# Kernel tuning notes

Measured on AMD Instinct MI355X. Metric: run time of the kernel, lower is better.

The kernel has to match this reference:

```python
import jax, jax.numpy as jnp
import numpy as np

NUM_CLASSES = 2
LOG2_NC = float(np.log2(NUM_CLASSES))


def _conv(x, w, b=None):
    # NCHW conv, stride 1, SAME padding (kernel 3 pad 1 or kernel 1 pad 0)
    y = jax.lax.conv_general_dilated(x, w, (1, 1), 'SAME',
                                     dimension_numbers=('NCHW', 'OIHW', 'NCHW'))
    if b is not None:
        y = y + b[None, :, None, None]
    return y


def _uncertainty_map(ds):
    # entropy over class dim, thresholded to {0,1}
    logp = jax.nn.log_softmax(ds, axis=1)            # [B,C,H,W]
    prob = jnp.exp(logp)
    # torch uses log2(prob + 1e-6); replicate exactly
    ent = -jnp.sum(prob * jnp.log2(prob + 1e-6), axis=1) / LOG2_NC  # [B,H,W]
    return (ent >= 0.001).astype(jnp.float32)


def _unob(tar, amap):
    # vectorized UnoB with S=3: interior pixels with tar!=0 get pro=0 unless
    # 4*tar == sum of the 4-neighborhood (i.e. locally constant label)
    t = tar  # [B,H,W] int
    nb = t[:, 2:, 1:-1] + t[:, :-2, 1:-1] + t[:, 1:-1, 2:] + t[:, 1:-1, :-2]
    center = t[:, 1:-1, 1:-1]
    inner_pro = jnp.where((center != 0) & (4 * center != nb), 0.0, 1.0)
    pro = jnp.ones_like(amap)
    pro = pro.at[:, 1:-1, 1:-1].set(inner_pro)
    return amap * pro


def setup_inputs() -> dict:
    key = jax.random.key(0)
    ks = jax.random.split(key, 6)
    B, C, H, W = 8, 128, 128, 128
    return {
        'x': jax.random.normal(ks[0], (B, C, H, W), jnp.float32),
        'skip': jax.random.normal(ks[1], (B, C, H, W), jnp.float32),
        'tar': jax.random.randint(ks[2], (B, 1, H, W), 0, NUM_CLASSES, jnp.int64)
            if jax.config.jax_enable_x64 else
            jax.random.randint(ks[2], (B, 1, H, W), 0, NUM_CLASSES).astype(jnp.int32),
        'W1': jax.random.normal(ks[3], (128, 256, 3, 3), jnp.float32) * 0.05,
        'b1': jnp.zeros((128,), jnp.float32),
        'W2': jax.random.normal(ks[4], (128, 128, 3, 3), jnp.float32) * 0.05,
        'b2': jnp.zeros((128,), jnp.float32),
        'Wds': jax.random.normal(ks[5], (NUM_CLASSES, 128, 1, 1), jnp.float32) * 0.05,
    }


def reference(x, skip, tar, W1, b1, W2, b2, Wds):
    h = jnp.concatenate([x, skip], axis=1)            # [B,2*dim,H,W]
    h = jax.nn.leaky_relu(_conv(h, W1, b1), 0.01)     # [B,dim,H,W]
    h = jax.nn.leaky_relu(_conv(h, W2, b2), 0.01)
    ds = _conv(h, Wds)                                # [B,num_classes,H,W]
    amap = _uncertainty_map(ds)                       # [B,H,W]
    amap = _unob(tar[:, 0], amap)                     # UnoB refinement, S=3
    return h, ds, amap
```

## Files before the change

kernel.cpp:

```cpp
#include <hip/hip_runtime.h>

typedef float f32x16 __attribute__((ext_vector_type(16)));
typedef short bf16x8 __attribute__((ext_vector_type(8)));
typedef unsigned int u32;

static __device__ __forceinline__ unsigned short f2bf(float f) {
  union { float f; unsigned int u; } v;
  v.f = f;
  return (unsigned short)((v.u + 0x7FFFu + ((v.u >> 16) & 1u)) >> 16);
}

static __device__ __forceinline__ void gl_lds16(const unsigned short* g,
                                                unsigned short* l) {
  __builtin_amdgcn_global_load_lds(
      (const __attribute__((address_space(1))) u32*)g,
      (__attribute__((address_space(3))) u32*)l, 16, 0, 0);
}

__global__ __launch_bounds__(256) void convert_weights(
    const float* __restrict__ W1, const float* __restrict__ W2,
    unsigned short* __restrict__ W1b, unsigned short* __restrict__ W2b,
    unsigned short* __restrict__ zp) {
  if (blockIdx.x == 1728) {
    uint4* z = (uint4*)zp;
    z[threadIdx.x] = make_uint4(0, 0, 0, 0);
    z[256 + threadIdx.x] = make_uint4(0, 0, 0, 0);
    return;
  }
  int i = blockIdx.x * 256 + threadIdx.x;
  if (i < 294912) {
    int e = i & 7, co = (i >> 3) & 127, r = i >> 10;
    int tap = r % 9, pc = r / 9;
    int ci = (pc >> 1) * 16 + (pc & 1) * 8 + e;
    W1b[i] = f2bf(W1[(co * 256 + ci) * 9 + tap]);
  } else {
    int j = i - 294912;
    if (j < 147456) {
      int e = j & 7, co = (j >> 3) & 127, r = j >> 10;
      int tap = r % 9, pc = r / 9;
      int ci = (pc >> 1) * 16 + (pc & 1) * 8 + e;
      W2b[j] = f2bf(W2[(co * 128 + ci) * 9 + tap]);
    }
  }
}

__global__ __launch_bounds__(256) void transpose_to_bf16(
    const float* __restrict__ src, unsigned short* __restrict__ dst, int cigb) {
  int row = blockIdx.x;
  int b = row >> 7, y = row & 127;
  const float* s = src + (long)b * 128 * 16384 + (long)y * 128;
  for (int it = 0; it < 8; ++it) {
    int u = it * 256 + (int)threadIdx.x;
    int cig = u >> 7, px = u & 127;
    unsigned short pk[8];
#pragma unroll
    for (int e = 0; e < 8; ++e)
      pk[e] = f2bf(s[(long)(cig * 8 + e) * 16384 + px]);
    uint4 vv;
    vv.x = (unsigned)pk[0] | ((unsigned)pk[1] << 16);
    vv.y = (unsigned)pk[2] | ((unsigned)pk[3] << 16);
    vv.z = (unsigned)pk[4] | ((unsigned)pk[5] << 16);
    vv.w = (unsigned)pk[6] | ((unsigned)pk[7] << 16);
    *(uint4*)(&dst[(((long)row * 32 + cigb + cig) * 130 + px + 1) * 8]) = vv;
  }
  if (cigb == 0 && threadIdx.x < 64) {
    int g = threadIdx.x >> 1;
    long col = (threadIdx.x & 1) * 129L;
    *(uint4*)(&dst[(((long)row * 32 + g) * 130 + col) * 8]) = make_uint4(0, 0, 0, 0);
  }
}

#define IPL 520
template <int CIN, bool FUSE_DS>
__global__ __launch_bounds__(512) void conv3x3(
    const unsigned short* __restrict__ src,
    const unsigned short* __restrict__ wt,
    const float* __restrict__ bias,
    const unsigned short* __restrict__ zp,
    unsigned short* __restrict__ dst_bf16,
    float* __restrict__ dst_f32,
    const float* __restrict__ wds,
    const int* __restrict__ tar,
    float* __restrict__ ds,
    float* __restrict__ amap) {
  constexpr int CPG = CIN / 8;
  constexpr int NC = CIN / 16;
  __shared__ unsigned short in_tile[2][2 * IPL * 8];
  __shared__ unsigned short wt_tile[2][2304 * 8];
  __shared__ float sb[128];
  __shared__ float w0s[128], w1s[128];
  __shared__ float sc[4 * 2 * 2 * 32];

  const int tid = threadIdx.x;
  const int b = blockIdx.x >> 6;
  const int y0 = (blockIdx.x & 63) * 2;
  const int lane = tid & 63, wave = tid >> 6;
  const int wco = wave & 1, wpx = wave >> 1;
  const int l31 = lane & 31, kh = lane >> 5;
  const int rowoff = wpx >> 1, p0 = (wpx & 1) * 64;

  if (tid < 128) {
    sb[tid] = bias[tid];
    if constexpr (FUSE_DS) {
      w0s[tid] = wds[tid];
      w1s[tid] = wds[128 + tid];
    }
  }

  const int shy = wave >> 1, sp = wave & 1;
  const int sgy = y0 - 1 + shy;
  const bool sok = (sgy >= 0 && sgy < 128);
  const unsigned short* srow =
      sok ? src + ((long)((b * 128 + sgy) * CPG) + sp) * 1040 : zp;
  const int tseg = tid >> 1, thx = 128 + (tid & 1);
  const int tp = tseg & 1, thy = tseg >> 1;
  const int tgy = y0 - 1 + thy;

#define STAGE_WT(cic, bufi)                                                   \
  {                                                                           \
    const unsigned short* wslab = wt + (long)(cic)*18432;                     \
    for (int o = wave; o < 36; o += 8)                                        \
      gl_lds16(wslab + (o * 64 + lane) * 8,                                   \
               &wt_tile[bufi][(size_t)(o * 64) * 8]);                         \
  }

#define STAGE_BULK(cic, bufi)                                                 \
  {                                                                           \
    _Pragma("unroll") for (int j = 0; j < 2; ++j)                             \
        gl_lds16(srow + (sok ? ((long)(cic)*2 * 1040 + (j * 64 + lane) * 8)   \
                             : (long)(lane * 8)),                             \
                 &in_tile[bufi][(size_t)(sp * IPL + shy * 130 + j * 64) * 8]);\
  }

#define LOAD_TAIL(cic, v)                                                     \
  {                                                                           \
    if (tid < 16 && tgy >= 0 && tgy < 128)                                    \
      v = *(const uint4*)(src +                                               \
                          ((long)((b * 128 + tgy) * CPG) + (cic)*2 + tp) *    \
                              1040 +                                          \
                          thx * 8);                                           \
  }

#define WRITE_TAIL(bufi, v)                                                   \
  {                                                                           \
    if (tid < 16)                                                             \
      *(uint4*)(&in_tile[bufi][(size_t)(tp * IPL + thy * 130 + thx) * 8]) = v;\
  }

  f32x16 acc[2][2] = {};

  {
    uint4 tv = make_uint4(0, 0, 0, 0);
    LOAD_TAIL(0, tv);
    STAGE_WT(0, 0);
    STAGE_BULK(0, 0);
    WRITE_TAIL(0, tv);
  }
  __syncthreads();

  for (int cic = 0; cic < NC; ++cic) {
    const int cur = cic & 1, nb = cur ^ 1;
    const bool more = (cic + 1 < NC);
    uint4 tl = make_uint4(0, 0, 0, 0);
    if (more) {
      LOAD_TAIL(cic + 1, tl);
      STAGE_WT(cic + 1, nb);
      STAGE_BULK(cic + 1, nb);
    }
    __builtin_amdgcn_sched_barrier(0);
    const unsigned short* it = in_tile[cur];
    const unsigned short* wl = wt_tile[cur];
    const size_t ibase = (size_t)(kh * IPL) * 8;
    const size_t wbase = (size_t)(kh * 1152) * 8;
#pragma unroll
    for (int ky = 0; ky < 3; ++ky) {
      const int hy = ky + rowoff;
#pragma unroll
      for (int kx = 0; kx < 3; ++kx) {
        const int t = ky * 3 + kx;
        bf16x8 a0 = *(const bf16x8*)(&wl[wbase + (size_t)(t * 128 + wco * 64 + l31) * 8]);
        bf16x8 a1 = *(const bf16x8*)(&wl[wbase + (size_t)(t * 128 + wco * 64 + 32 + l31) * 8]);
        bf16x8 b0 = *(const bf16x8*)(&it[ibase + (size_t)(hy * 130 + p0 + l31 + kx) * 8]);
        bf16x8 b1 = *(const bf16x8*)(&it[ibase + (size_t)(hy * 130 + p0 + 32 + l31 + kx) * 8]);
        acc[0][0] = __builtin_amdgcn_mfma_f32_32x32x16_bf16(a0, b0, acc[0][0], 0, 0, 0);
        acc[0][1] = __builtin_amdgcn_mfma_f32_32x32x16_bf16(a0, b1, acc[0][1], 0, 0, 0);
        acc[1][0] = __builtin_amdgcn_mfma_f32_32x32x16_bf16(a1, b0, acc[1][0], 0, 0, 0);
        acc[1][1] = __builtin_amdgcn_mfma_f32_32x32x16_bf16(a1, b1, acc[1][1], 0, 0, 0);
      }
    }
    if (more) WRITE_TAIL(nb, tl);
    __syncthreads();
  }

  const int gyo = y0 + rowoff;
  float pd[2][2] = {};
#pragma unroll
  for (int fc = 0; fc < 2; ++fc) {
#pragma unroll
    for (int fp = 0; fp < 2; ++fp) {
      const int px = p0 + fp * 32 + l31;
      if constexpr (!FUSE_DS) {
#pragma unroll
        for (int rg = 0; rg < 4; ++rg) {
          const int co0 = wco * 64 + fc * 32 + rg * 8 + kh * 4;
          unsigned short pk[4];
#pragma unroll
          for (int q = 0; q < 4; ++q) {
            float v = acc[fc][fp][rg * 4 + q] + sb[co0 + q];
            v = v > 0.f ? v : 0.01f * v;
            pk[q] = f2bf(v);
          }
          uint2 o;
          o.x = (unsigned)pk[0] | ((unsigned)pk[1] << 16);
          o.y = (unsigned)pk[2] | ((unsigned)pk[3] << 16);
          *(uint2*)(&dst_bf16[(((long)(b * 128 + gyo) * 16 + (co0 >> 3)) * 130 + px + 1) * 8 +
                              kh * 4]) = o;
        }
      } else {
#pragma unroll
        for (int rg = 0; rg < 4; ++rg) {
          const int co0 = wco * 64 + fc * 32 + rg * 8 + kh * 4;
          float4 wv0 = *(const float4*)(&w0s[co0]);
          float4 wv1 = *(const float4*)(&w1s[co0]);
#pragma unroll
          for (int q = 0; q < 4; ++q) {
            float v = acc[fc][fp][rg * 4 + q] + sb[co0 + q];
            v = v > 0.f ? v : 0.01f * v;
            dst_f32[((long)(b * 128 + co0 + q) << 14) + (gyo << 7) + px] = v;
            float wq0 = (q == 0) ? wv0.x : (q == 1) ? wv0.y : (q == 2) ? wv0.z : wv0.w;
            float wq1 = (q == 0) ? wv1.x : (q == 1) ? wv1.y : (q == 2) ? wv1.z : wv1.w;
            pd[fp][0] += wq0 * v;
            pd[fp][1] += wq1 * v;
          }
        }
      }
    }
  }

  if constexpr (!FUSE_DS) {
    if (tid < 64) {
      int row = tid >> 5, g = (tid >> 1) & 15;
      long col = (tid & 1) * 129L;
      *(uint4*)(&dst_bf16[(((long)(b * 128 + y0 + row) * 16 + g) * 130 + col) * 8]) =
          make_uint4(0, 0, 0, 0);
    }
  } else {
#pragma unroll
    for (int fp = 0; fp < 2; ++fp)
#pragma unroll
      for (int c = 0; c < 2; ++c)
        pd[fp][c] += __shfl_xor(pd[fp][c], 32, 64);
    if (wco == 1 && kh == 0) {
#pragma unroll
      for (int fp = 0; fp < 2; ++fp)
#pragma unroll
        for (int c = 0; c < 2; ++c)
          sc[((wpx * 2 + fp) * 2 + c) * 32 + l31] = pd[fp][c];
    }
    __syncthreads();
    if (wco == 0 && kh == 0) {
      const int* tb = tar + (long)b * 16384;
#pragma unroll
      for (int fp = 0; fp < 2; ++fp) {
        const int px = p0 + fp * 32 + l31;
        float a0 = pd[fp][0] + sc[((wpx * 2 + fp) * 2 + 0) * 32 + l31];
        float a1 = pd[fp][1] + sc[((wpx * 2 + fp) * 2 + 1) * 32 + l31];
        ds[((long)b * 2) * 16384 + (gyo << 7) + px] = a0;
        ds[((long)b * 2 + 1) * 16384 + (gyo << 7) + px] = a1;
        float m = fmaxf(a0, a1);
        float e0 = expf(a0 - m), e1 = expf(a1 - m);
        float s = e0 + e1;
        float p0f = e0 / s, p1f = e1 / s;
        float ent = -(p0f * log2f(p0f + 1e-6f) + p1f * log2f(p1f + 1e-6f));
        float un = ent >= 0.001f ? 1.f : 0.f;
        float pro = 1.f;
        if (gyo > 0 && gyo < 127 && px > 0 && px < 127) {
          int c = tb[(gyo << 7) + px];
          if (c != 0) {
            int nb2 = tb[((gyo - 1) << 7) + px] + tb[((gyo + 1) << 7) + px] +
                      tb[(gyo << 7) + px - 1] + tb[(gyo << 7) + px + 1];
            if (4 * c != nb2) pro = 0.f;
          }
        }
        amap[((long)(b * 128 + gyo) << 7) + px] = un * pro;
      }
    }
  }
#undef STAGE_WT
#undef STAGE_BULK
#undef LOAD_TAIL
#undef WRITE_TAIL
}

extern "C" void kernel_launch(void* const* d_in, const int* in_sizes, int n_in,
                              void* d_out, int out_size, void* d_ws, size_t ws_size,
                              hipStream_t stream) {
  const float* x    = (const float*)d_in[0];
  const float* skip = (const float*)d_in[1];
  const int*   tar  = (const int*)d_in[2];
  const float* W1   = (const float*)d_in[3];
  const float* b1   = (const float*)d_in[4];
  const float* W2   = (const float*)d_in[5];
  const float* b2   = (const float*)d_in[6];
  const float* Wds  = (const float*)d_in[7];

  float* out_h  = (float*)d_out;
  float* out_ds = out_h + 16777216;
  float* out_am = out_ds + 262144;

  unsigned short* W1b = (unsigned short*)d_ws;
  unsigned short* W2b = W1b + 294912;
  unsigned short* zp  = W2b + 147456;
  unsigned short* h1  = (unsigned short*)((char*)d_ws + (1u << 20));

  unsigned short* h0 = (unsigned short*)d_out;

  convert_weights<<<1729, 256, 0, stream>>>(W1, W2, W1b, W2b, zp);
  transpose_to_bf16<<<1024, 256, 0, stream>>>(x, h0, 0);
  transpose_to_bf16<<<1024, 256, 0, stream>>>(skip, h0, 16);
  conv3x3<256, false><<<512, 512, 0, stream>>>(h0, W1b, b1, zp, h1, nullptr,
                                               nullptr, nullptr, nullptr, nullptr);
  conv3x3<128, true><<<512, 512, 0, stream>>>(h1, W2b, b2, zp, nullptr, out_h,
                                              Wds, tar, out_ds, out_am);
}
```

Before: 163.8 us.

## Shrink conv tiles to one row per block and stream weights from global

The conv3x3 kernel now handles one output row per 256-thread block, with a 1024-block grid instead of 512 blocks of 512 threads. Weights are no longer staged through shared memory; each lane reads its weight fragments straight from global (L2) with a one-ky-ahead register prefetch. This cuts LDS use to allow several blocks per CU (launch bounds 256,3) and drops the weight-staging traffic and its barrier cost. In exchange every block re-reads the weights from cache, input halo rows are reused less (3 rows loaded per output row instead of 4 per 2), and register pressure from the prefetched fragments rises.

```diff
diff --git a/kernel.cpp b/kernel.cpp
--- a/kernel.cpp
+++ b/kernel.cpp
@@ -70,9 +70,8 @@
   }
 }
 
-#define IPL 520
 template <int CIN, bool FUSE_DS>
-__global__ __launch_bounds__(512) void conv3x3(
+__global__ __launch_bounds__(256, 3) void conv3x3(
     const unsigned short* __restrict__ src,
     const unsigned short* __restrict__ wt,
     const float* __restrict__ bias,
@@ -85,19 +84,18 @@
     float* __restrict__ amap) {
   constexpr int CPG = CIN / 8;
   constexpr int NC = CIN / 16;
-  __shared__ unsigned short in_tile[2][2 * IPL * 8];
-  __shared__ unsigned short wt_tile[2][2304 * 8];
+  __shared__ unsigned short in_tile[2][6 * 130 * 8];
   __shared__ float sb[128];
   __shared__ float w0s[128], w1s[128];
-  __shared__ float sc[4 * 2 * 2 * 32];
+  __shared__ float sc[2 * 2 * 2 * 32];
 
   const int tid = threadIdx.x;
-  const int b = blockIdx.x >> 6;
-  const int y0 = (blockIdx.x & 63) * 2;
+  const int b = blockIdx.x >> 7;
+  const int y0 = blockIdx.x & 127;
   const int lane = tid & 63, wave = tid >> 6;
   const int wco = wave & 1, wpx = wave >> 1;
   const int l31 = lane & 31, kh = lane >> 5;
-  const int rowoff = wpx >> 1, p0 = (wpx & 1) * 64;
+  const int p0 = wpx * 64;
 
   if (tid < 128) {
     sb[tid] = bias[tid];
@@ -107,44 +105,42 @@
     }
   }
 
-  const int shy = wave >> 1, sp = wave & 1;
-  const int sgy = y0 - 1 + shy;
-  const bool sok = (sgy >= 0 && sgy < 128);
-  const unsigned short* srow =
-      sok ? src + ((long)((b * 128 + sgy) * CPG) + sp) * 1040 : zp;
-  const int tseg = tid >> 1, thx = 128 + (tid & 1);
-  const int tp = tseg & 1, thy = tseg >> 1;
-  const int tgy = y0 - 1 + thy;
-
-#define STAGE_WT(cic, bufi)                                                   \
-  {                                                                           \
-    const unsigned short* wslab = wt + (long)(cic)*18432;                     \
-    for (int o = wave; o < 36; o += 8)                                        \
-      gl_lds16(wslab + (o * 64 + lane) * 8,                                   \
-               &wt_tile[bufi][(size_t)(o * 64) * 8]);                         \
-  }
-
-#define STAGE_BULK(cic, bufi)                                                 \
-  {                                                                           \
-    _Pragma("unroll") for (int j = 0; j < 2; ++j)                             \
-        gl_lds16(srow + (sok ? ((long)(cic)*2 * 1040 + (j * 64 + lane) * 8)   \
-                             : (long)(lane * 8)),                             \
-                 &in_tile[bufi][(size_t)(sp * IPL + shy * 130 + j * 64) * 8]);\
-  }
-
-#define LOAD_TAIL(cic, v)                                                     \
-  {                                                                           \
-    if (tid < 16 && tgy >= 0 && tgy < 128)                                    \
-      v = *(const uint4*)(src +                                               \
-                          ((long)((b * 128 + tgy) * CPG) + (cic)*2 + tp) *    \
-                              1040 +                                          \
-                          thx * 8);                                           \
-  }
-
-#define WRITE_TAIL(bufi, v)                                                   \
-  {                                                                           \
-    if (tid < 16)                                                             \
-      *(uint4*)(&in_tile[bufi][(size_t)(tp * IPL + thy * 130 + thx) * 8]) = v;\
+#define STAGE_BULK(cic, bufi)                                                  \
+  {                                                                            \
+    _Pragma("unroll") for (int j = 0; j < 3; ++j) {                            \
+      int o = wave + j * 4;                                                    \
+      int seg = o >> 1, half = o & 1;                                          \
+      int p = (seg >= 3) ? 1 : 0, hy = seg - p * 3;                            \
+      int gy = y0 - 1 + hy;                                                    \
+      const unsigned short* g =                                                \
+          (gy >= 0 && gy < 128)                                                \
+              ? src + ((size_t)((b * 128 + gy) * CPG) + (cic)*2 + p) * 1040 +  \
+                    (half * 64 + lane) * 8                                     \
+              : zp + lane * 8;                                                 \
+      gl_lds16(g, &in_tile[bufi][(size_t)(seg * 130 + half * 64) * 8]);        \
+    }                                                                          \
+  }
+
+#define LOAD_TAIL(cic, v)                                                      \
+  {                                                                            \
+    if (tid < 12) {                                                            \
+      int s_ = tid >> 1, p_ = (s_ >= 3) ? 1 : 0, hy_ = s_ - p_ * 3;            \
+      int cx_ = 128 + (tid & 1);                                               \
+      int gy_ = y0 - 1 + hy_;                                                  \
+      if (gy_ >= 0 && gy_ < 128)                                               \
+        v = *(const uint4*)(src +                                              \
+                            ((size_t)((b * 128 + gy_) * CPG) + (cic)*2 + p_) * \
+                                1040 +                                         \
+                            cx_ * 8);                                          \
+    }                                                                          \
+  }
+
+#define WRITE_TAIL(bufi, v)                                                    \
+  {                                                                            \
+    if (tid < 12) {                                                            \
+      int s_ = tid >> 1, cx_ = 128 + (tid & 1);                                \
+      *(uint4*)(&in_tile[bufi][(size_t)(s_ * 130 + cx_) * 8]) = v;             \
+    }                                                                          \
   }
 
   f32x16 acc[2][2] = {};
@@ -152,47 +148,58 @@
   {
     uint4 tv = make_uint4(0, 0, 0, 0);
     LOAD_TAIL(0, tv);
-    STAGE_WT(0, 0);
     STAGE_BULK(0, 0);
     WRITE_TAIL(0, tv);
   }
   __syncthreads();
 
+  const unsigned short* wlane = wt + (size_t)kh * 9216 + (size_t)(wco * 64 + l31) * 8;
+
   for (int cic = 0; cic < NC; ++cic) {
-    const int cur = cic & 1, nb = cur ^ 1;
+    const int cur = cic & 1, nbuf = cur ^ 1;
     const bool more = (cic + 1 < NC);
     uint4 tl = make_uint4(0, 0, 0, 0);
     if (more) {
       LOAD_TAIL(cic + 1, tl);
-      STAGE_WT(cic + 1, nb);
-      STAGE_BULK(cic + 1, nb);
+      STAGE_BULK(cic + 1, nbuf);
     }
     __builtin_amdgcn_sched_barrier(0);
+    const unsigned short* wl = wlane + (size_t)cic * 18432;
     const unsigned short* it = in_tile[cur];
-    const unsigned short* wl = wt_tile[cur];
-    const size_t ibase = (size_t)(kh * IPL) * 8;
-    const size_t wbase = (size_t)(kh * 1152) * 8;
+    bf16x8 a0[3], a1[3];
+#pragma unroll
+    for (int t = 0; t < 3; ++t) {
+      a0[t] = *(const bf16x8*)(wl + t * 1024);
+      a1[t] = *(const bf16x8*)(wl + t * 1024 + 256);
+    }
 #pragma unroll
     for (int ky = 0; ky < 3; ++ky) {
-      const int hy = ky + rowoff;
+      bf16x8 n0[3], n1[3];
+      if (ky < 2) {
+#pragma unroll
+        for (int t = 0; t < 3; ++t) {
+          n0[t] = *(const bf16x8*)(wl + (ky * 3 + 3 + t) * 1024);
+          n1[t] = *(const bf16x8*)(wl + (ky * 3 + 3 + t) * 1024 + 256);
+        }
+      }
 #pragma unroll
       for (int kx = 0; kx < 3; ++kx) {
-        const int t = ky * 3 + kx;
-        bf16x8 a0 = *(const bf16x8*)(&wl[wbase + (size_t)(t * 128 + wco * 64 + l31) * 8]);
-        bf16x8 a1 = *(const bf16x8*)(&wl[wbase + (size_t)(t * 128 + wco * 64 + 32 + l31) * 8]);
-        bf16x8 b0 = *(const bf16x8*)(&it[ibase + (size_t)(hy * 130 + p0 + l31 + kx) * 8]);
-        bf16x8 b1 = *(const bf16x8*)(&it[ibase + (size_t)(hy * 130 + p0 + 32 + l31 + kx) * 8]);
-        acc[0][0] = __builtin_amdgcn_mfma_f32_32x32x16_bf16(a0, b0, acc[0][0], 0, 0, 0);
-        acc[0][1] = __builtin_amdgcn_mfma_f32_32x32x16_bf16(a0, b1, acc[0][1], 0, 0, 0);
-        acc[1][0] = __builtin_amdgcn_mfma_f32_32x32x16_bf16(a1, b0, acc[1][0], 0, 0, 0);
-        acc[1][1] = __builtin_amdgcn_mfma_f32_32x32x16_bf16(a1, b1, acc[1][1], 0, 0, 0);
-      }
-    }
-    if (more) WRITE_TAIL(nb, tl);
+        bf16x8 b0 = *(const bf16x8*)(&it[(size_t)(kh * 390 + ky * 130 + p0 + l31 + kx) * 8]);
+        bf16x8 b1 = *(const bf16x8*)(&it[(size_t)(kh * 390 + ky * 130 + p0 + 32 + l31 + kx) * 8]);
+        acc[0][0] = __builtin_amdgcn_mfma_f32_32x32x16_bf16(a0[kx], b0, acc[0][0], 0, 0, 0);
+        acc[0][1] = __builtin_amdgcn_mfma_f32_32x32x16_bf16(a0[kx], b1, acc[0][1], 0, 0, 0);
+        acc[1][0] = __builtin_amdgcn_mfma_f32_32x32x16_bf16(a1[kx], b0, acc[1][0], 0, 0, 0);
+        acc[1][1] = __builtin_amdgcn_mfma_f32_32x32x16_bf16(a1[kx], b1, acc[1][1], 0, 0, 0);
+      }
+      if (ky < 2) {
+#pragma unroll
+        for (int t = 0; t < 3; ++t) { a0[t] = n0[t]; a1[t] = n1[t]; }
+      }
+    }
+    if (more) WRITE_TAIL(nbuf, tl);
     __syncthreads();
   }
 
-  const int gyo = y0 + rowoff;
   float pd[2][2] = {};
 #pragma unroll
   for (int fc = 0; fc < 2; ++fc) {
@@ -213,7 +220,7 @@
           uint2 o;
           o.x = (unsigned)pk[0] | ((unsigned)pk[1] << 16);
           o.y = (unsigned)pk[2] | ((unsigned)pk[3] << 16);
-          *(uint2*)(&dst_bf16[(((long)(b * 128 + gyo) * 16 + (co0 >> 3)) * 130 + px + 1) * 8 +
+          *(uint2*)(&dst_bf16[(((long)(b * 128 + y0) * 16 + (co0 >> 3)) * 130 + px + 1) * 8 +
                               kh * 4]) = o;
         }
       } else {
@@ -226,7 +233,7 @@
           for (int q = 0; q < 4; ++q) {
             float v = acc[fc][fp][rg * 4 + q] + sb[co0 + q];
             v = v > 0.f ? v : 0.01f * v;
-            dst_f32[((long)(b * 128 + co0 + q) << 14) + (gyo << 7) + px] = v;
+            dst_f32[((long)(b * 128 + co0 + q) << 14) + (y0 << 7) + px] = v;
             float wq0 = (q == 0) ? wv0.x : (q == 1) ? wv0.y : (q == 2) ? wv0.z : wv0.w;
             float wq1 = (q == 0) ? wv1.x : (q == 1) ? wv1.y : (q == 2) ? wv1.z : wv1.w;
             pd[fp][0] += wq0 * v;
@@ -238,10 +245,10 @@
   }
 
   if constexpr (!FUSE_DS) {
-    if (tid < 64) {
-      int row = tid >> 5, g = (tid >> 1) & 15;
+    if (tid < 32) {
+      int g = tid >> 1;
       long col = (tid & 1) * 129L;
-      *(uint4*)(&dst_bf16[(((long)(b * 128 + y0 + row) * 16 + g) * 130 + col) * 8]) =
+      *(uint4*)(&dst_bf16[(((long)(b * 128 + y0) * 16 + g) * 130 + col) * 8]) =
           make_uint4(0, 0, 0, 0);
     }
   } else {
@@ -265,8 +272,8 @@
         const int px = p0 + fp * 32 + l31;
         float a0 = pd[fp][0] + sc[((wpx * 2 + fp) * 2 + 0) * 32 + l31];
         float a1 = pd[fp][1] + sc[((wpx * 2 + fp) * 2 + 1) * 32 + l31];
-        ds[((long)b * 2) * 16384 + (gyo << 7) + px] = a0;
-        ds[((long)b * 2 + 1) * 16384 + (gyo << 7) + px] = a1;
+        ds[((long)b * 2) * 16384 + (y0 << 7) + px] = a0;
+        ds[((long)b * 2 + 1) * 16384 + (y0 << 7) + px] = a1;
         float m = fmaxf(a0, a1);
         float e0 = expf(a0 - m), e1 = expf(a1 - m);
         float s = e0 + e1;
@@ -274,19 +281,18 @@
         float ent = -(p0f * log2f(p0f + 1e-6f) + p1f * log2f(p1f + 1e-6f));
         float un = ent >= 0.001f ? 1.f : 0.f;
         float pro = 1.f;
-        if (gyo > 0 && gyo < 127 && px > 0 && px < 127) {
-          int c = tb[(gyo << 7) + px];
+        if (y0 > 0 && y0 < 127 && px > 0 && px < 127) {
+          int c = tb[(y0 << 7) + px];
           if (c != 0) {
-            int nb2 = tb[((gyo - 1) << 7) + px] + tb[((gyo + 1) << 7) + px] +
-                      tb[(gyo << 7) + px - 1] + tb[(gyo << 7) + px + 1];
+            int nb2 = tb[((y0 - 1) << 7) + px] + tb[((y0 + 1) << 7) + px] +
+                      tb[(y0 << 7) + px - 1] + tb[(y0 << 7) + px + 1];
             if (4 * c != nb2) pro = 0.f;
           }
         }
-        amap[((long)(b * 128 + gyo) << 7) + px] = un * pro;
-      }
-    }
-  }
-#undef STAGE_WT
+        amap[((long)(b * 128 + y0) << 7) + px] = un * pro;
+      }
+    }
+  }
 #undef STAGE_BULK
 #undef LOAD_TAIL
 #undef WRITE_TAIL
@@ -318,8 +324,8 @@
   convert_weights<<<1729, 256, 0, stream>>>(W1, W2, W1b, W2b, zp);
   transpose_to_bf16<<<1024, 256, 0, stream>>>(x, h0, 0);
   transpose_to_bf16<<<1024, 256, 0, stream>>>(skip, h0, 16);
-  conv3x3<256, false><<<512, 512, 0, stream>>>(h0, W1b, b1, zp, h1, nullptr,
-                                               nullptr, nullptr, nullptr, nullptr);
-  conv3x3<128, true><<<512, 512, 0, stream>>>(h1, W2b, b2, zp, nullptr, out_h,
-                                              Wds, tar, out_ds, out_am);
-}
+  conv3x3<256, false><<<1024, 256, 0, stream>>>(h0, W1b, b1, zp, h1, nullptr,
+                                                nullptr, nullptr, nullptr, nullptr);
+  conv3x3<128, true><<<1024, 256, 0, stream>>>(h1, W2b, b2, zp, nullptr, out_h,
+                                               Wds, tar, out_ds, out_am);
+}
```

Result: slower. 192.9 us (+17.8%).

## Use 4-wave blocks with larger per-wave tiles and single-buffered weight staging

Applied to the files above, without the earlier changes.

The conv3x3 kernel drops from 8 waves to 4 waves per block, and each wave now computes a full 128-pixel row (a 2x4 MFMA tile instead of 2x2). This doubles B-fragment reuse per A load and cuts redundant LDS reads. Weights are now staged into a single LDS buffer each iteration, and the input keeps its double buffer. Synchronisation uses explicit vmcnt/lgkmcnt waits and raw barriers. The aim is to reduce LDS traffic and shared-memory footprint so two blocks fit per CU, at the cost of doubling accumulator registers. Weight loads are no longer prefetched ahead, which may expose global latency.

```diff
diff --git a/kernel.cpp b/kernel.cpp
--- a/kernel.cpp
+++ b/kernel.cpp
@@ -16,6 +16,12 @@
       (const __attribute__((address_space(1))) u32*)g,
       (__attribute__((address_space(3))) u32*)l, 16, 0, 0);
 }
+
+#define VMCNT4 asm volatile("s_waitcnt vmcnt(4)" ::: "memory")
+#define VMCNT0 asm volatile("s_waitcnt vmcnt(0)" ::: "memory")
+#define LGKM0 asm volatile("s_waitcnt lgkmcnt(0)" ::: "memory")
+#define BAR __builtin_amdgcn_s_barrier()
+#define SCHEDB __builtin_amdgcn_sched_barrier(0)
 
 __global__ __launch_bounds__(256) void convert_weights(
     const float* __restrict__ W1, const float* __restrict__ W2,
@@ -70,9 +76,8 @@
   }
 }
 
-#define IPL 520
 template <int CIN, bool FUSE_DS>
-__global__ __launch_bounds__(512) void conv3x3(
+__global__ __launch_bounds__(256, 2) void conv3x3(
     const unsigned short* __restrict__ src,
     const unsigned short* __restrict__ wt,
     const float* __restrict__ bias,
@@ -85,19 +90,18 @@
     float* __restrict__ amap) {
   constexpr int CPG = CIN / 8;
   constexpr int NC = CIN / 16;
-  __shared__ unsigned short in_tile[2][2 * IPL * 8];
-  __shared__ unsigned short wt_tile[2][2304 * 8];
+  __shared__ unsigned short in_tile[2][1040 * 8];
+  __shared__ unsigned short wt_tile[2304 * 8];
   __shared__ float sb[128];
   __shared__ float w0s[128], w1s[128];
-  __shared__ float sc[4 * 2 * 2 * 32];
+  __shared__ float sc[2 * 4 * 2 * 32];
 
   const int tid = threadIdx.x;
   const int b = blockIdx.x >> 6;
   const int y0 = (blockIdx.x & 63) * 2;
   const int lane = tid & 63, wave = tid >> 6;
-  const int wco = wave & 1, wpx = wave >> 1;
+  const int wco = wave & 1, wrow = wave >> 1;
   const int l31 = lane & 31, kh = lane >> 5;
-  const int rowoff = wpx >> 1, p0 = (wpx & 1) * 64;
 
   if (tid < 128) {
     sb[tid] = bias[tid];
@@ -107,98 +111,123 @@
     }
   }
 
-  const int shy = wave >> 1, sp = wave & 1;
-  const int sgy = y0 - 1 + shy;
-  const bool sok = (sgy >= 0 && sgy < 128);
-  const unsigned short* srow =
-      sok ? src + ((long)((b * 128 + sgy) * CPG) + sp) * 1040 : zp;
-  const int tseg = tid >> 1, thx = 128 + (tid & 1);
-  const int tp = tseg & 1, thy = tseg >> 1;
-  const int tgy = y0 - 1 + thy;
-
-#define STAGE_WT(cic, bufi)                                                   \
-  {                                                                           \
-    const unsigned short* wslab = wt + (long)(cic)*18432;                     \
-    for (int o = wave; o < 36; o += 8)                                        \
-      gl_lds16(wslab + (o * 64 + lane) * 8,                                   \
-               &wt_tile[bufi][(size_t)(o * 64) * 8]);                         \
-  }
-
-#define STAGE_BULK(cic, bufi)                                                 \
-  {                                                                           \
-    _Pragma("unroll") for (int j = 0; j < 2; ++j)                             \
-        gl_lds16(srow + (sok ? ((long)(cic)*2 * 1040 + (j * 64 + lane) * 8)   \
-                             : (long)(lane * 8)),                             \
-                 &in_tile[bufi][(size_t)(sp * IPL + shy * 130 + j * 64) * 8]);\
-  }
-
-#define LOAD_TAIL(cic, v)                                                     \
-  {                                                                           \
-    if (tid < 16 && tgy >= 0 && tgy < 128)                                    \
-      v = *(const uint4*)(src +                                               \
-                          ((long)((b * 128 + tgy) * CPG) + (cic)*2 + tp) *    \
-                              1040 +                                          \
-                          thx * 8);                                           \
-  }
-
-#define WRITE_TAIL(bufi, v)                                                   \
-  {                                                                           \
-    if (tid < 16)                                                             \
-      *(uint4*)(&in_tile[bufi][(size_t)(tp * IPL + thy * 130 + thx) * 8]) = v;\
-  }
-
-  f32x16 acc[2][2] = {};
+#define STAGE_IN(cic, bufi)                                                    \
+  {                                                                            \
+    _Pragma("unroll") for (int j = 0; j < 4; ++j) {                            \
+      int o = wave * 4 + j;                                                    \
+      int s = o * 64 + lane;                                                   \
+      int p = s >= 520;                                                        \
+      int r = s - p * 520;                                                     \
+      int hy = r / 130;                                                        \
+      int hx = r - hy * 130;                                                   \
+      int gy = y0 - 1 + hy;                                                    \
+      const unsigned short* g =                                                \
+          (gy >= 0 && gy < 128)                                                \
+              ? src + ((size_t)((b * 128 + gy) * CPG) + (size_t)(cic)*2 + p) * \
+                          1040 +                                               \
+                    hx * 8                                                     \
+              : zp + lane * 8;                                                 \
+      gl_lds16(g, &in_tile[bufi][(size_t)o * 512]);                            \
+    }                                                                          \
+  }
+
+#define STAGE_WT(cic)                                                          \
+  {                                                                            \
+    const unsigned short* wslab = wt + (size_t)(cic)*18432;                    \
+    _Pragma("unroll") for (int j = 0; j < 9; ++j) {                            \
+      int o = wave * 9 + j;                                                    \
+      gl_lds16(wslab + o * 512 + lane * 8, &wt_tile[(size_t)o * 512]);         \
+    }                                                                          \
+  }
+
+#define LOAD_TAIL(cic, v)                                                      \
+  {                                                                            \
+    if (tid < 16) {                                                            \
+      int gy_ = y0 + 2;                                                        \
+      if (gy_ < 128)                                                           \
+        v = *(const uint4*)(src +                                              \
+                            ((size_t)((b * 128 + gy_) * CPG) +                 \
+                             (size_t)(cic)*2 + 1) *                            \
+                                1040 +                                         \
+                            (114 + tid) * 8);                                  \
+    }                                                                          \
+  }
+
+#define WRITE_TAIL(bufi, v)                                                    \
+  {                                                                            \
+    if (tid < 16) *(uint4*)(&in_tile[bufi][(size_t)(1024 + tid) * 8]) = v;     \
+  }
+
+  f32x16 acc[2][4] = {};
 
   {
     uint4 tv = make_uint4(0, 0, 0, 0);
     LOAD_TAIL(0, tv);
-    STAGE_WT(0, 0);
-    STAGE_BULK(0, 0);
+    STAGE_IN(0, 0);
+    VMCNT0;
     WRITE_TAIL(0, tv);
-  }
-  __syncthreads();
+    LGKM0;
+    BAR;
+    SCHEDB;
+  }
 
   for (int cic = 0; cic < NC; ++cic) {
-    const int cur = cic & 1, nb = cur ^ 1;
+    const int cur = cic & 1;
     const bool more = (cic + 1 < NC);
     uint4 tl = make_uint4(0, 0, 0, 0);
+    if (more) LOAD_TAIL(cic + 1, tl);
+    STAGE_WT(cic);
     if (more) {
-      LOAD_TAIL(cic + 1, tl);
-      STAGE_WT(cic + 1, nb);
-      STAGE_BULK(cic + 1, nb);
-    }
-    __builtin_amdgcn_sched_barrier(0);
+      STAGE_IN(cic + 1, cur ^ 1);
+      VMCNT4;
+      SCHEDB;
+      WRITE_TAIL(cur ^ 1, tl);
+    } else {
+      VMCNT0;
+      SCHEDB;
+    }
+    LGKM0;
+    BAR;
+    SCHEDB;
+
     const unsigned short* it = in_tile[cur];
-    const unsigned short* wl = wt_tile[cur];
-    const size_t ibase = (size_t)(kh * IPL) * 8;
-    const size_t wbase = (size_t)(kh * 1152) * 8;
+    const size_t wb = (size_t)kh * 9216;
+    const size_t ib = (size_t)kh * 4160;
 #pragma unroll
     for (int ky = 0; ky < 3; ++ky) {
-      const int hy = ky + rowoff;
+      const int hy = ky + wrow;
 #pragma unroll
       for (int kx = 0; kx < 3; ++kx) {
         const int t = ky * 3 + kx;
-        bf16x8 a0 = *(const bf16x8*)(&wl[wbase + (size_t)(t * 128 + wco * 64 + l31) * 8]);
-        bf16x8 a1 = *(const bf16x8*)(&wl[wbase + (size_t)(t * 128 + wco * 64 + 32 + l31) * 8]);
-        bf16x8 b0 = *(const bf16x8*)(&it[ibase + (size_t)(hy * 130 + p0 + l31 + kx) * 8]);
-        bf16x8 b1 = *(const bf16x8*)(&it[ibase + (size_t)(hy * 130 + p0 + 32 + l31 + kx) * 8]);
+        bf16x8 a0 = *(const bf16x8*)(&wt_tile[wb + (size_t)(t * 128 + wco * 64 + l31) * 8]);
+        bf16x8 a1 = *(const bf16x8*)(&wt_tile[wb + (size_t)(t * 128 + wco * 64 + 32 + l31) * 8]);
+        bf16x8 b0 = *(const bf16x8*)(&it[ib + (size_t)(hy * 130 + l31 + kx) * 8]);
+        bf16x8 b1 = *(const bf16x8*)(&it[ib + (size_t)(hy * 130 + 32 + l31 + kx) * 8]);
+        bf16x8 b2 = *(const bf16x8*)(&it[ib + (size_t)(hy * 130 + 64 + l31 + kx) * 8]);
+        bf16x8 b3 = *(const bf16x8*)(&it[ib + (size_t)(hy * 130 + 96 + l31 + kx) * 8]);
         acc[0][0] = __builtin_amdgcn_mfma_f32_32x32x16_bf16(a0, b0, acc[0][0], 0, 0, 0);
         acc[0][1] = __builtin_amdgcn_mfma_f32_32x32x16_bf16(a0, b1, acc[0][1], 0, 0, 0);
+        acc[0][2] = __builtin_amdgcn_mfma_f32_32x32x16_bf16(a0, b2, acc[0][2], 0, 0, 0);
+        acc[0][3] = __builtin_amdgcn_mfma_f32_32x32x16_bf16(a0, b3, acc[0][3], 0, 0, 0);
         acc[1][0] = __builtin_amdgcn_mfma_f32_32x32x16_bf16(a1, b0, acc[1][0], 0, 0, 0);
         acc[1][1] = __builtin_amdgcn_mfma_f32_32x32x16_bf16(a1, b1, acc[1][1], 0, 0, 0);
+        acc[1][2] = __builtin_amdgcn_mfma_f32_32x32x16_bf16(a1, b2, acc[1][2], 0, 0, 0);
+        acc[1][3] = __builtin_amdgcn_mfma_f32_32x32x16_bf16(a1, b3, acc[1][3], 0, 0, 0);
       }
     }
-    if (more) WRITE_TAIL(nb, tl);
-    __syncthreads();
-  }
-
-  const int gyo = y0 + rowoff;
-  float pd[2][2] = {};
+    SCHEDB;
+    LGKM0;
+    BAR;
+    SCHEDB;
+  }
+
+  const int gyo = y0 + wrow;
+  float pd[4][2] = {};
 #pragma unroll
   for (int fc = 0; fc < 2; ++fc) {
 #pragma unroll
-    for (int fp = 0; fp < 2; ++fp) {
-      const int px = p0 + fp * 32 + l31;
+    for (int fp = 0; fp < 4; ++fp) {
+      const int px = fp * 32 + l31;
       if constexpr (!FUSE_DS) {
 #pragma unroll
         for (int rg = 0; rg < 4; ++rg) {
@@ -246,25 +275,25 @@
     }
   } else {
 #pragma unroll
-    for (int fp = 0; fp < 2; ++fp)
+    for (int fp = 0; fp < 4; ++fp)
 #pragma unroll
       for (int c = 0; c < 2; ++c)
         pd[fp][c] += __shfl_xor(pd[fp][c], 32, 64);
     if (wco == 1 && kh == 0) {
 #pragma unroll
-      for (int fp = 0; fp < 2; ++fp)
+      for (int fp = 0; fp < 4; ++fp)
 #pragma unroll
         for (int c = 0; c < 2; ++c)
-          sc[((wpx * 2 + fp) * 2 + c) * 32 + l31] = pd[fp][c];
+          sc[((wrow * 4 + fp) * 2 + c) * 32 + l31] = pd[fp][c];
     }
     __syncthreads();
     if (wco == 0 && kh == 0) {
       const int* tb = tar + (long)b * 16384;
 #pragma unroll
-      for (int fp = 0; fp < 2; ++fp) {
-        const int px = p0 + fp * 32 + l31;
-        float a0 = pd[fp][0] + sc[((wpx * 2 + fp) * 2 + 0) * 32 + l31];
-        float a1 = pd[fp][1] + sc[((wpx * 2 + fp) * 2 + 1) * 32 + l31];
+      for (int fp = 0; fp < 4; ++fp) {
+        const int px = fp * 32 + l31;
+        float a0 = pd[fp][0] + sc[((wrow * 4 + fp) * 2 + 0) * 32 + l31];
+        float a1 = pd[fp][1] + sc[((wrow * 4 + fp) * 2 + 1) * 32 + l31];
         ds[((long)b * 2) * 16384 + (gyo << 7) + px] = a0;
         ds[((long)b * 2 + 1) * 16384 + (gyo << 7) + px] = a1;
         float m = fmaxf(a0, a1);
@@ -286,8 +315,8 @@
       }
     }
   }
+#undef STAGE_IN
 #undef STAGE_WT
-#undef STAGE_BULK
 #undef LOAD_TAIL
 #undef WRITE_TAIL
 }
@@ -318,8 +347,8 @@
   convert_weights<<<1729, 256, 0, stream>>>(W1, W2, W1b, W2b, zp);
   transpose_to_bf16<<<1024, 256, 0, stream>>>(x, h0, 0);
   transpose_to_bf16<<<1024, 256, 0, stream>>>(skip, h0, 16);
-  conv3x3<256, false><<<512, 512, 0, stream>>>(h0, W1b, b1, zp, h1, nullptr,
+  conv3x3<256, false><<<512, 256, 0, stream>>>(h0, W1b, b1, zp, h1, nullptr,
                                                nullptr, nullptr, nullptr, nullptr);
-  conv3x3<128, true><<<512, 512, 0, stream>>>(h1, W2b, b2, zp, nullptr, out_h,
+  conv3x3<128, true><<<512, 256, 0, stream>>>(h1, W2b, b2, zp, nullptr, out_h,
                                               Wds, tar, out_ds, out_am);
 }
```

Measured after the change: 154.9 us. -5.4%, faster.
